# Optimization experiments

Measured on AMD Instinct MI355X. Metric: run time of the kernel, lower is better.

## Reference

```python
import jax, jax.numpy as jnp
import numpy as np

B, CIN, COUT, RES, WDIM, K = 16, 512, 512, 64, 512, 3
LRELU_ALPHA = 0.2
ACT_GAIN = float(np.sqrt(2.0))  # bias_act def_gain for lrelu


def setup_inputs() -> dict:
    key = jax.random.key(0)
    ks = jax.random.split(key, 8)
    return {
        "x": jax.random.normal(ks[0], (B, CIN, RES, RES), dtype=jnp.float32),
        "w": jax.random.normal(ks[1], (B, WDIM), dtype=jnp.float32),
        "weight": jax.random.normal(ks[2], (COUT, CIN, K, K), dtype=jnp.float32),
        "bias": jnp.zeros((COUT,), dtype=jnp.float32),
        "affine_w": jax.random.normal(ks[3], (CIN, WDIM), dtype=jnp.float32),
        "affine_b": jnp.ones((CIN,), dtype=jnp.float32),  # bias_init=1
        "noise_const": jax.random.normal(ks[4], (RES, RES), dtype=jnp.float32),
        "noise_strength": jnp.asarray(0.1, dtype=jnp.float32),
    }


def reference(x, w, weight, bias, affine_w, affine_b, noise_const, noise_strength):
    # affine: FullyConnectedLayer with lr-equalized weight scale 1/sqrt(w_dim)
    styles = w @ (affine_w.T * (1.0 / np.sqrt(WDIM))) + affine_b  # [B, CIN]

    # modulate: per-sample scaled weights [B, COUT, CIN, K, K]
    wmod = weight[None] * styles[:, None, :, None, None]
    # demodulate
    demod = jax.lax.rsqrt(jnp.sum(wmod * wmod, axis=(2, 3, 4)) + 1e-8)  # [B, COUT]
    wmod = wmod * demod[:, :, None, None, None]

    # per-sample conv2d, padding=k//2 (StyleGAN2 groups=batch trick -> vmap)
    def conv1(xi, wi):
        return jax.lax.conv_general_dilated(
            xi[None], wi, window_strides=(1, 1),
            padding=[(K // 2, K // 2), (K // 2, K // 2)],
            dimension_numbers=("NCHW", "OIHW", "NCHW"))[0]

    y = jax.vmap(conv1)(x, wmod)  # [B, COUT, RES, RES]

    # noise injection (noise_mode='const'): broadcast [RES,RES] over batch/channel
    y = y + noise_const * noise_strength

    # fused bias + lrelu + gain (conv_clamp=None)
    y = y + bias[None, :, None, None]
    y = jnp.where(y >= 0, y, LRELU_ALPHA * y) * ACT_GAIN
    return y
```

## Files before the change

kernel.cpp:

```cpp
#include <hip/hip_runtime.h>
#include <hip/hip_bf16.h>

#define B_     16
#define CIN_   512
#define COUT_  512
#define RES_   64
#define WDIM_  512
#define LRELU_A 0.2f
#define GAIN_  1.4142135623730951f

typedef __attribute__((ext_vector_type(8)))  __bf16 bf16x8;
typedef __attribute__((ext_vector_type(16))) float  f32x16;
typedef __attribute__((ext_vector_type(4)))  int    int4v;

__device__ __forceinline__ unsigned short f2bf(float f) {
    union { float f; unsigned int u; } v; v.f = f;
    unsigned int u = v.u;
    return (unsigned short)((u + 0x7FFFu + ((u >> 16) & 1u)) >> 16);
}

__device__ __forceinline__ void gl_lds16(const void* g, void* l) {
    __builtin_amdgcn_global_load_lds(
        (const __attribute__((address_space(1))) unsigned int*)g,
        (__attribute__((address_space(3))) unsigned int*)l, 16, 0, 0);
}

__global__ void zero_k(unsigned short* __restrict__ xs) {
    int idx = blockIdx.x * 256 + threadIdx.x;
    int b = idx >> 13, side = (idx >> 12) & 1, off = idx & 4095;
    int4v z = {0, 0, 0, 0};
    *(int4v*)((char*)xs + ((size_t)(b * 66 + side * 65) * 4096 + off) * 16) = z;
}

__global__ void styles_k(const float* __restrict__ w, const float* __restrict__ aw,
                         const float* __restrict__ ab, float* __restrict__ styles) {
    int idx = blockIdx.x * 256 + threadIdx.x;
    int b = idx >> 9, ci = idx & 511;
    const float4* wp = (const float4*)(w + b * WDIM_);
    const float4* ap = (const float4*)(aw + (size_t)ci * WDIM_);
    float acc = 0.f;
    #pragma unroll 4
    for (int k = 0; k < WDIM_ / 4; ++k) {
        float4 a = ap[k], q = wp[k];
        acc += a.x * q.x + a.y * q.y + a.z * q.z + a.w * q.w;
    }
    styles[idx] = acc * 0.04419417382415922f + ab[ci];
}

__global__ void wprep_k(const float* __restrict__ weight, unsigned short* __restrict__ wt,
                        float* __restrict__ wsq) {
    int idx = blockIdx.x * 256 + threadIdx.x;
    int co = idx >> 9, ci = idx & 511;
    const float* wp = weight + (size_t)idx * 9;
    float s = 0.f;
    #pragma unroll
    for (int t = 0; t < 9; ++t) {
        float f = wp[t];
        s += f * f;
        wt[(((size_t)(ci >> 4) * 9 + t) * 512 + co) * 16 + (ci & 15)] = f2bf(f);
    }
    wsq[idx] = s;
}

__global__ void demod_k(const float* __restrict__ styles, const float* __restrict__ wsq,
                        float* __restrict__ demod) {
    int idx = blockIdx.x * 256 + threadIdx.x;
    int b = idx >> 9, co = idx & 511;
    const float4* wr = (const float4*)(wsq + (size_t)co * CIN_);
    const float4* sr = (const float4*)(styles + (size_t)b * CIN_);
    float acc = 0.f;
    #pragma unroll 4
    for (int ci = 0; ci < CIN_ / 4; ++ci) {
        float4 q = wr[ci], s = sr[ci];
        acc += q.x * s.x * s.x + q.y * s.y * s.y + q.z * s.z * s.z + q.w * s.w * s.w;
    }
    demod[idx] = rsqrtf(acc + 1e-8f);
}

__global__ void xprep_k(const float* __restrict__ x, const float* __restrict__ styles,
                        unsigned short* __restrict__ xs) {
    __shared__ float tile[64][65];
    int bid = blockIdx.x;
    int ct = bid & 7, h = (bid >> 3) & 63, b = bid >> 9;
    int tw = threadIdx.x & 63;
    int tr = threadIdx.x >> 6;
    const float* xp = x + (((size_t)(b * CIN_ + ct * 64) * RES_ + h) * RES_);
    #pragma unroll
    for (int it = 0; it < 16; ++it) {
        int ci = tr + it * 4;
        tile[ci][tw] = xp[(size_t)ci * (RES_ * RES_) + tw];
    }
    __syncthreads();
    const float sv = styles[b * CIN_ + ct * 64 + tw];
    unsigned short* xo = xs + (size_t)(b * 66 + h + 1) * 32768
                            + ((size_t)(ct * 4 + (tw >> 4))) * 1024 + (tw & 15);
    #pragma unroll
    for (int it = 0; it < 16; ++it) {
        int w = tr + it * 4;
        xo[w * 16] = f2bf(tile[tw][w] * sv);
    }
}

#define WBUF 36864
#define XBUF 21120
#define LDS_TOTAL (2*WBUF + 2*XBUF)

__global__ __launch_bounds__(512, 2) void conv_k(
    const unsigned short* __restrict__ xs, const unsigned short* __restrict__ wt,
    const float* __restrict__ demod, const float* __restrict__ bias,
    const float* __restrict__ noise, const float* __restrict__ nsp,
    float* __restrict__ out)
{
    extern __shared__ char lds[];
    char* Wl = lds;
    char* Xl = lds + 2 * WBUF;

    const int tid  = threadIdx.x;
    const int lane = tid & 63;
    const int wid  = tid >> 6;
    const int l31  = lane & 31;
    const int kg   = lane >> 5;

    const int lb = ((blockIdx.x & 7) << 6) | (blockIdx.x >> 3);
    const int m  = lb >> 7;
    const int pt = lb & 127;
    const int b  = pt >> 3;
    const int h0 = (pt & 7) * 8;

    if (tid < 80) {
        int buf = tid / 40, rem = tid % 40, r = rem >> 2, k = rem & 3;
        int chunk = r * 132 + (k < 2 ? k : 128 + k);
        int4v z = {0, 0, 0, 0};
        *(int4v*)(Xl + buf * XBUF + chunk * 16) = z;
    }

    const char* wsrc = (const char*)wt + (size_t)m * (128 * 32);
    auto stageW = [&](int cc, int buf) {
        const char* s0 = wsrc + (size_t)cc * (9 * 512 * 32);
        char* d0 = Wl + buf * WBUF;
        #pragma unroll
        for (int k = 0; k < 5; ++k) {
            if (k < 4 || wid < 4) {
                const int c0 = k * 512 + wid * 64;
                const int c  = c0 + lane;
                gl_lds16(s0 + (size_t)(c >> 8) * 16384 + (c & 255) * 16, d0 + c0 * 16);
            }
        }
    };
    const char* xsrc = (const char*)xs + (size_t)(b * 66 + h0) * 65536;
    auto stageX = [&](int cc, int buf) {
        const char* s0 = xsrc + cc * 2048;
        char* d0 = Xl + buf * XBUF;
        #pragma unroll
        for (int k = 0; k < 3; ++k) {
            if (k < 2 || wid < 4) {
                const int c0 = k * 512 + wid * 64;
                const int c  = c0 + lane;
                const int r  = c0 >> 7;
                gl_lds16(s0 + (size_t)r * 65536 + (c & 127) * 16,
                         d0 + r * 2112 + ((c0 & 127) + 2) * 16);
            }
        }
    };

    f32x16 acc[4][2];
    #pragma unroll
    for (int mt = 0; mt < 4; ++mt)
        #pragma unroll
        for (int nt = 0; nt < 2; ++nt)
            #pragma unroll
            for (int j = 0; j < 16; ++j) acc[mt][nt][j] = 0.f;

    stageW(0, 0);
    stageX(0, 0);
    __syncthreads();

    int buf = 0;
    for (int cc = 0; cc < 32; ++cc) {
        if (cc < 31) { stageW(cc + 1, buf ^ 1); stageX(cc + 1, buf ^ 1); }
        const char* Wb = Wl + buf * WBUF;
        const char* Xb = Xl + buf * XBUF;
        #pragma unroll
        for (int t = 0; t < 9; ++t) {
            const int dy = t / 3, dx = t % 3;
            bf16x8 af[4], bv[2];
            #pragma unroll
            for (int mt = 0; mt < 4; ++mt)
                af[mt] = *(const bf16x8*)(Wb + ((t * 128 + mt * 32 + l31) << 5) + (kg << 4));
            #pragma unroll
            for (int nt = 0; nt < 2; ++nt) {
                int site = nt * 32 + l31 + dx;
                bv[nt] = *(const bf16x8*)(Xb + (wid + dy) * 2112 + site * 32 + (kg << 4));
            }
            #pragma unroll
            for (int mt = 0; mt < 4; ++mt)
                #pragma unroll
                for (int nt = 0; nt < 2; ++nt)
                    acc[mt][nt] = __builtin_amdgcn_mfma_f32_32x32x16_bf16(
                        af[mt], bv[nt], acc[mt][nt], 0, 0, 0);
        }
        __syncthreads();
        buf ^= 1;
    }

    const float nsv = nsp[0];
    const int h = h0 + wid;
    const float* dm = demod + b * COUT_ + m * 128;
    float nz[2];
    nz[0] = noise[h * 64 + l31] * nsv;
    nz[1] = noise[h * 64 + 32 + l31] * nsv;
    #pragma unroll
    for (int mt = 0; mt < 4; ++mt) {
        #pragma unroll
        for (int j = 0; j < 16; ++j) {
            int row = (j & 3) + 8 * (j >> 2) + 4 * kg;
            int co  = mt * 32 + row;
            float d  = dm[co];
            float bs = bias[m * 128 + co];
            #pragma unroll
            for (int nt = 0; nt < 2; ++nt) {
                float v = acc[mt][nt][j] * d + nz[nt] + bs;
                v = (v >= 0.f ? v : LRELU_A * v) * GAIN_;
                out[((size_t)(b * COUT_ + m * 128 + co) * RES_ + h) * RES_ + nt * 32 + l31] = v;
            }
        }
    }
}

extern "C" void kernel_launch(void* const* d_in, const int* in_sizes, int n_in,
                              void* d_out, int out_size, void* d_ws, size_t ws_size,
                              hipStream_t stream) {
    const float* x    = (const float*)d_in[0];
    const float* w    = (const float*)d_in[1];
    const float* wgt  = (const float*)d_in[2];
    const float* bias = (const float*)d_in[3];
    const float* aw   = (const float*)d_in[4];
    const float* ab   = (const float*)d_in[5];
    const float* noi  = (const float*)d_in[6];
    const float* ns   = (const float*)d_in[7];
    float* out = (float*)d_out;

    char* ws = (char*)d_ws;
    float* styles        = (float*)(ws);
    float* demod         = (float*)(ws + 32768);
    float* wsq           = (float*)(ws + 65536);
    unsigned short* wt   = (unsigned short*)(ws + 1114112);
    unsigned short* xs   = (unsigned short*)(ws + 6291456);

    hipLaunchKernelGGL(zero_k,   dim3(512),  dim3(256), 0, stream, xs);
    hipLaunchKernelGGL(styles_k, dim3(32),   dim3(256), 0, stream, w, aw, ab, styles);
    hipLaunchKernelGGL(wprep_k,  dim3(1024), dim3(256), 0, stream, wgt, wt, wsq);
    hipLaunchKernelGGL(xprep_k,  dim3(8192), dim3(256), 0, stream, x, styles, xs);
    hipLaunchKernelGGL(demod_k,  dim3(32),   dim3(256), 0, stream, styles, wsq, demod);

    hipFuncSetAttribute((const void*)conv_k, hipFuncAttributeMaxDynamicSharedMemorySize, LDS_TOTAL);
    hipLaunchKernelGGL(conv_k, dim3(512), dim3(512), LDS_TOTAL, stream,
                       xs, wt, demod, bias, noi, ns, out);
}
```

Baseline: 523.8 us.

## Shrink conv blocks, single-buffer weights with XOR swizzle, vectorize xprep

The conv kernel moves to 256-thread blocks covering 4 rows instead of 8, and the grid grows to 1024 blocks. Weights now sit in a single LDS buffer that is reloaded between barriers after each channel chunk, while X stays double-buffered. This frees LDS so more blocks can be resident per CU. An XOR swizzle on LDS addresses is meant to cut bank conflicts, and xprep now uses float4 loads and 16-byte bf16 stores. The cost is that the weight load is exposed as a serialized stall each iteration and is fetched twice as often across the grid.

```diff
diff --git a/kernel.cpp b/kernel.cpp
--- a/kernel.cpp
+++ b/kernel.cpp
@@ -12,6 +12,7 @@
 typedef __attribute__((ext_vector_type(8)))  __bf16 bf16x8;
 typedef __attribute__((ext_vector_type(16))) float  f32x16;
 typedef __attribute__((ext_vector_type(4)))  int    int4v;
+typedef __attribute__((ext_vector_type(8)))  unsigned short u16x8;
 
 __device__ __forceinline__ unsigned short f2bf(float f) {
     union { float f; unsigned int u; } v; v.f = f;
@@ -80,32 +81,38 @@
 __global__ void xprep_k(const float* __restrict__ x, const float* __restrict__ styles,
                         unsigned short* __restrict__ xs) {
     __shared__ float tile[64][65];
+    __shared__ float styv[64];
     int bid = blockIdx.x;
     int ct = bid & 7, h = (bid >> 3) & 63, b = bid >> 9;
-    int tw = threadIdx.x & 63;
-    int tr = threadIdx.x >> 6;
-    const float* xp = x + (((size_t)(b * CIN_ + ct * 64) * RES_ + h) * RES_);
-    #pragma unroll
-    for (int it = 0; it < 16; ++it) {
-        int ci = tr + it * 4;
-        tile[ci][tw] = xp[(size_t)ci * (RES_ * RES_) + tw];
+    int tid = threadIdx.x;
+    if (tid < 64) styv[tid] = styles[b * CIN_ + ct * 64 + tid];
+    const float* xp = x + (((size_t)(b * CIN_ + ct * 64)) * RES_ + h) * RES_;
+    #pragma unroll
+    for (int it = 0; it < 4; ++it) {
+        int ci = it * 16 + (tid >> 4);
+        int w4 = (tid & 15) * 4;
+        float4 v = *(const float4*)(xp + (size_t)ci * (RES_ * RES_) + w4);
+        tile[ci][w4] = v.x; tile[ci][w4 + 1] = v.y; tile[ci][w4 + 2] = v.z; tile[ci][w4 + 3] = v.w;
     }
     __syncthreads();
-    const float sv = styles[b * CIN_ + ct * 64 + tw];
-    unsigned short* xo = xs + (size_t)(b * 66 + h + 1) * 32768
-                            + ((size_t)(ct * 4 + (tw >> 4))) * 1024 + (tw & 15);
-    #pragma unroll
-    for (int it = 0; it < 16; ++it) {
-        int w = tr + it * 4;
-        xo[w * 16] = f2bf(tile[tw][w] * sv);
+    unsigned short* xo = xs + (size_t)(b * 66 + h + 1) * 32768 + (size_t)ct * 4096;
+    #pragma unroll
+    for (int it = 0; it < 2; ++it) {
+        int s = it * 256 + tid;
+        int ccl = s >> 7, w = (s >> 1) & 63, half = s & 1;
+        int ci0 = ccl * 16 + half * 8;
+        u16x8 v;
+        #pragma unroll
+        for (int j = 0; j < 8; ++j) v[j] = f2bf(tile[ci0 + j][w] * styv[ci0 + j]);
+        *(u16x8*)(xo + ccl * 1024 + w * 16 + half * 8) = v;
     }
 }
 
 #define WBUF 36864
-#define XBUF 21120
-#define LDS_TOTAL (2*WBUF + 2*XBUF)
-
-__global__ __launch_bounds__(512, 2) void conv_k(
+#define XBUF 12672
+#define LDS_TOTAL (WBUF + 2*XBUF)
+
+__global__ __launch_bounds__(256, 2) void conv_k(
     const unsigned short* __restrict__ xs, const unsigned short* __restrict__ wt,
     const float* __restrict__ demod, const float* __restrict__ bias,
     const float* __restrict__ noise, const float* __restrict__ nsp,
@@ -113,7 +120,7 @@
 {
     extern __shared__ char lds[];
     char* Wl = lds;
-    char* Xl = lds + 2 * WBUF;
+    char* Xl = lds + WBUF;
 
     const int tid  = threadIdx.x;
     const int lane = tid & 63;
@@ -121,30 +128,29 @@
     const int l31  = lane & 31;
     const int kg   = lane >> 5;
 
-    const int lb = ((blockIdx.x & 7) << 6) | (blockIdx.x >> 3);
-    const int m  = lb >> 7;
-    const int pt = lb & 127;
-    const int b  = pt >> 3;
-    const int h0 = (pt & 7) * 8;
-
-    if (tid < 80) {
-        int buf = tid / 40, rem = tid % 40, r = rem >> 2, k = rem & 3;
+    const int lb = ((blockIdx.x & 7) << 7) | (blockIdx.x >> 3);
+    const int m  = lb >> 8;
+    const int rest = lb & 255;
+    const int b  = rest >> 4;
+    const int h0 = (rest & 15) * 4;
+
+    if (tid < 48) {
+        int buf = tid / 24, rem = tid % 24, r = rem >> 2, k = rem & 3;
         int chunk = r * 132 + (k < 2 ? k : 128 + k);
         int4v z = {0, 0, 0, 0};
         *(int4v*)(Xl + buf * XBUF + chunk * 16) = z;
     }
 
     const char* wsrc = (const char*)wt + (size_t)m * (128 * 32);
-    auto stageW = [&](int cc, int buf) {
+    auto stageW = [&](int cc) {
         const char* s0 = wsrc + (size_t)cc * (9 * 512 * 32);
-        char* d0 = Wl + buf * WBUF;
-        #pragma unroll
-        for (int k = 0; k < 5; ++k) {
-            if (k < 4 || wid < 4) {
-                const int c0 = k * 512 + wid * 64;
-                const int c  = c0 + lane;
-                gl_lds16(s0 + (size_t)(c >> 8) * 16384 + (c & 255) * 16, d0 + c0 * 16);
-            }
+        #pragma unroll
+        for (int k = 0; k < 9; ++k) {
+            const int c0 = k * 256 + (wid << 6);
+            const int c  = c0 + lane;
+            const int sc = c ^ ((c >> 3) & 1);
+            gl_lds16(s0 + (size_t)(sc >> 8) * 16384 + (size_t)(sc & 255) * 16,
+                     Wl + c0 * 16);
         }
     };
     const char* xsrc = (const char*)xs + (size_t)(b * 66 + h0) * 65536;
@@ -153,13 +159,12 @@
         char* d0 = Xl + buf * XBUF;
         #pragma unroll
         for (int k = 0; k < 3; ++k) {
-            if (k < 2 || wid < 4) {
-                const int c0 = k * 512 + wid * 64;
-                const int c  = c0 + lane;
-                const int r  = c0 >> 7;
-                gl_lds16(s0 + (size_t)r * 65536 + (c & 127) * 16,
-                         d0 + r * 2112 + ((c0 & 127) + 2) * 16);
-            }
+            const int c0 = k * 256 + (wid << 6);
+            const int r  = c0 >> 7;
+            const int cw = ((c0 + lane) & 127) + 2;
+            const int sw = cw ^ ((cw >> 3) & 1);
+            gl_lds16(s0 + (size_t)r * 65536 + (size_t)(sw - 2) * 16,
+                     d0 + (r * 132 + ((c0 & 127) + 2)) * 16);
         }
     };
 
@@ -171,26 +176,31 @@
             #pragma unroll
             for (int j = 0; j < 16; ++j) acc[mt][nt][j] = 0.f;
 
-    stageW(0, 0);
+    stageW(0);
     stageX(0, 0);
+    asm volatile("s_waitcnt vmcnt(0)" ::: "memory");
     __syncthreads();
 
-    int buf = 0;
+    int xb = 0;
     for (int cc = 0; cc < 32; ++cc) {
-        if (cc < 31) { stageW(cc + 1, buf ^ 1); stageX(cc + 1, buf ^ 1); }
-        const char* Wb = Wl + buf * WBUF;
-        const char* Xb = Xl + buf * XBUF;
+        if (cc < 31) stageX(cc + 1, xb ^ 1);
+        const char* Xb = Xl + xb * XBUF;
         #pragma unroll
         for (int t = 0; t < 9; ++t) {
             const int dy = t / 3, dx = t % 3;
             bf16x8 af[4], bv[2];
             #pragma unroll
-            for (int mt = 0; mt < 4; ++mt)
-                af[mt] = *(const bf16x8*)(Wb + ((t * 128 + mt * 32 + l31) << 5) + (kg << 4));
+            for (int mt = 0; mt < 4; ++mt) {
+                int o = (mt * 32 + l31) * 32 + (kg << 4);
+                o ^= (o >> 3) & 16;
+                af[mt] = *(const bf16x8*)(Wl + t * 4096 + o);
+            }
             #pragma unroll
             for (int nt = 0; nt < 2; ++nt) {
                 int site = nt * 32 + l31 + dx;
-                bv[nt] = *(const bf16x8*)(Xb + (wid + dy) * 2112 + site * 32 + (kg << 4));
+                int o = site * 32 + (kg << 4);
+                o ^= (o >> 3) & 16;
+                bv[nt] = *(const bf16x8*)(Xb + (wid + dy) * 2112 + o);
             }
             #pragma unroll
             for (int mt = 0; mt < 4; ++mt)
@@ -199,8 +209,15 @@
                     acc[mt][nt] = __builtin_amdgcn_mfma_f32_32x32x16_bf16(
                         af[mt], bv[nt], acc[mt][nt], 0, 0, 0);
         }
-        __syncthreads();
-        buf ^= 1;
+        if (cc < 31) {
+            __builtin_amdgcn_sched_barrier(0);
+            __builtin_amdgcn_s_barrier();
+            stageW(cc + 1);
+            asm volatile("s_waitcnt vmcnt(0)" ::: "memory");
+            __builtin_amdgcn_s_barrier();
+            __builtin_amdgcn_sched_barrier(0);
+        }
+        xb ^= 1;
     }
 
     const float nsv = nsp[0];
@@ -254,6 +271,6 @@
     hipLaunchKernelGGL(demod_k,  dim3(32),   dim3(256), 0, stream, styles, wsq, demod);
 
     hipFuncSetAttribute((const void*)conv_k, hipFuncAttributeMaxDynamicSharedMemorySize, LDS_TOTAL);
-    hipLaunchKernelGGL(conv_k, dim3(512), dim3(512), LDS_TOTAL, stream,
+    hipLaunchKernelGGL(conv_k, dim3(1024), dim3(256), LDS_TOTAL, stream,
                        xs, wt, demod, bias, noi, ns, out);
 }
```

Result: no change. 528.4 us (+0.9%).
